# Kernel optimization log

Measured on AMD Instinct MI355X. Metric: run time of the kernel, lower is better.

## Reference

```python
import jax, jax.numpy as jnp
import numpy as np
from math import factorial, sqrt, pi

# ---- static config (matches init_kwargs) ----
C = 64            # channel multiplicity of hidden irreps 64x0e+64x1o+64x2e
L_HID = 2
MAX_ELL = 3
N_BASIS = 8
R_MAX = 5.0
AVG_NEI = 16.0
NUM_SPECIES = 5
N_NODES = 10000
N_EDGES = 160000
RAD_HID = 64
DIMS = [2 * l + 1 for l in range(L_HID + 1)]   # [1,3,5]

# ---- Clebsch-Gordan coefficients in the real spherical-harmonic basis ----
def _cg(j1, m1, j2, m2, j3, m3):
    if m1 + m2 != m3:
        return 0.0
    f = factorial
    pref = sqrt((2 * j3 + 1) * f(j3 + j1 - j2) * f(j3 - j1 + j2) * f(j1 + j2 - j3) / f(j1 + j2 + j3 + 1))
    pref *= sqrt(f(j3 + m3) * f(j3 - m3) * f(j1 - m1) * f(j1 + m1) * f(j2 - m2) * f(j2 + m2))
    s = 0.0
    for k in range(j1 + j2 - j3 + 1):
        d = (k, j1 + j2 - j3 - k, j1 - m1 - k, j2 + m2 - k, j3 - j2 + m1 + k, j3 - j1 - m2 + k)
        if min(d) < 0:
            continue
        s += (-1.0) ** k / np.prod([float(f(x)) for x in d])
    return pref * s

def _real_basis(l):
    A = np.zeros((2 * l + 1, 2 * l + 1), dtype=complex)
    for mp in range(-l, l + 1):
        if mp > 0:
            A[l + mp, l + mp] = (-1) ** mp / sqrt(2); A[l + mp, l - mp] = 1 / sqrt(2)
        elif mp == 0:
            A[l, l] = 1.0
        else:
            m = -mp
            A[l + mp, l - m] = 1j / sqrt(2); A[l + mp, l + m] = -1j * (-1) ** m / sqrt(2)
    return A

def _real_cg(l1, l2, l3):
    Cc = np.zeros((2 * l1 + 1, 2 * l2 + 1, 2 * l3 + 1), dtype=complex)
    for a in range(-l1, l1 + 1):
        for b in range(-l2, l2 + 1):
            c = a + b
            if -l3 <= c <= l3:
                Cc[l1 + a, l2 + b, l3 + c] = _cg(l1, a, l2, b, l3, c)
    A1, A2, A3 = _real_basis(l1), _real_basis(l2), _real_basis(l3)
    Cr = np.einsum('ia,jb,kc,abc->ijk', A1, A2, A3.conj(), Cc)
    R = Cr.real if np.abs(Cr.real).sum() >= np.abs(Cr.imag).sum() else Cr.imag
    R = R / max(np.sqrt((R ** 2).sum()), 1e-12)   # path-normalized
    return jnp.asarray(R.astype(np.float32))

def _paths(ls_in):
    ps = []
    for l1 in ls_in:
        for l2 in range(MAX_ELL + 1):
            for l3 in range(L_HID + 1):
                # triangle inequality + parity match (hidden parities are (-1)^l, SH parity (-1)^l)
                if abs(l1 - l2) <= l3 <= l1 + l2 and (l1 + l2 + l3) % 2 == 0:
                    ps.append((l1, l2, l3))
    return ps

PATHS = [_paths([0]), _paths(list(range(L_HID + 1)))]   # layer 0: 3 paths, layer 1: 13 paths
CG = {p: _real_cg(*p) for layer in PATHS for p in layer}

# ---- real spherical harmonics up to l=3 (component-style normalization) ----
def sph_harm(u):
    x, y, z = u[:, 0], u[:, 1], u[:, 2]
    Y0 = jnp.ones_like(x)[:, None]
    Y1 = sqrt(3.0) * jnp.stack([y, z, x], -1)
    Y2 = jnp.stack([sqrt(15) * x * y, sqrt(15) * y * z, sqrt(5) / 2 * (3 * z * z - 1),
                    sqrt(15) * x * z, sqrt(15) / 2 * (x * x - y * y)], -1)
    Y3 = jnp.stack([sqrt(35 / 8) * y * (3 * x * x - y * y), sqrt(105) * x * y * z,
                    sqrt(21 / 8) * y * (5 * z * z - 1), sqrt(7) / 2 * z * (5 * z * z - 3),
                    sqrt(21 / 8) * x * (5 * z * z - 1), sqrt(105) / 2 * z * (x * x - y * y),
                    sqrt(35 / 8) * x * (x * x - 3 * y * y)], -1)
    return [Y0, Y1, Y2, Y3]

def bessel(r):
    # e3nn.bessel(r, N_BASIS, R_MAX)
    n = jnp.arange(1, N_BASIS + 1, dtype=r.dtype)
    rs = jnp.maximum(r, 1e-6)[:, None]
    return sqrt(2.0 / R_MAX) * jnp.sin(n * pi * rs / R_MAX) / rs

def soft_envelope(r):
    # e3nn.soft_envelope: value_at_origin=1.2, arg_multiplicator=2.0
    t = 2.0 * (1.0 - r / R_MAX)
    sus = jnp.where(t > 0, jnp.exp(-1.0 / jnp.where(t > 0, t, 1.0)), 0.0)
    return (1.2 / np.exp(-0.5)) * sus

def interaction(h, Ys, rad, paths, rad_w1, rad_w2, mix, senders, receivers, n_nodes):
    # radial MLP -> per-path, per-channel tensor-product weights
    w = jax.nn.silu(rad @ rad_w1) @ rad_w2                       # [E, P*C]
    w = w.reshape(rad.shape[0], len(paths), C)
    hs = {l: h[l][senders] for l in {p[0] for p in paths}}       # gather once per input l
    acc = [None] * (L_HID + 1)
    for p, (l1, l2, l3) in enumerate(paths):
        # CG tensor product of sender features with edge spherical harmonics
        m = jnp.einsum('eci,ej,ijk,ec->eck', hs[l1], Ys[l2], CG[(l1, l2, l3)], w[:, p])
        acc[l3] = m if acc[l3] is None else acc[l3] + m
    out = {}
    for l in range(L_HID + 1):
        node_m = jax.ops.segment_sum(acc[l], receivers, num_segments=n_nodes) / AVG_NEI
        out[l] = jnp.einsum('nck,cd->ndk', node_m, mix[l])       # linear channel mixing per irrep
    return out

def forward(positions, w_embed, rad_w1_0, rad_w2_0, mix0, read0,
            rad_w1_1, rad_w2_1, mix1, skip1, read1, species, senders, receivers):
    n = positions.shape[0]
    rel = positions[receivers] - positions[senders]              # [E,3]
    r = jnp.sqrt(jnp.sum(rel * rel, -1) + 1e-12)
    u = rel / r[:, None]
    Ys = sph_harm(u)
    rad = bessel(r) * soft_envelope(r)[:, None]                  # [E,B]
    h = {0: w_embed[species][:, :, None]}                        # initial scalar node features
    # layer 0 (skip_connection_first_layer=False)
    h = interaction(h, Ys, rad, PATHS[0], rad_w1_0, rad_w2_0, mix0, senders, receivers, n)
    out0 = jnp.concatenate([jnp.einsum('nck,cd->ndk', h[l], read0[l]).reshape(n, -1)
                            for l in range(L_HID + 1)], -1)      # [N, C*9]
    # layer 1 (with linear skip connection)
    m = interaction(h, Ys, rad, PATHS[1], rad_w1_1, rad_w2_1, mix1, senders, receivers, n)
    h = {l: m[l] + jnp.einsum('nck,cd->ndk', h[l], skip1[l]) for l in range(L_HID + 1)}
    out1 = jnp.concatenate([jnp.einsum('nck,cd->ndk', h[l], read1[l]).reshape(n, -1)
                            for l in range(L_HID + 1)], -1)
    # per-layer readouts stacked then flattened == axis_to_mul over the layer axis
    return jnp.concatenate([out0, out1], -1)                     # [N, 2*C*9] = [N, 1152]

def setup_inputs() -> dict:
    key = jax.random.key(0)
    ks = jax.random.split(key, 14)
    P = [len(PATHS[0]), len(PATHS[1])]
    def w(k, shape, fan_in):
        return jax.random.normal(k, shape, jnp.float32) / np.sqrt(fan_in)
    return {
        'positions': jax.random.normal(ks[0], (N_NODES, 3), jnp.float32) * 1.5,
        'species': jax.random.randint(ks[1], (N_NODES,), 0, NUM_SPECIES),
        'senders': jax.random.randint(ks[2], (N_EDGES,), 0, N_NODES),
        'receivers': jax.random.randint(ks[3], (N_EDGES,), 0, N_NODES),
        'w_embed': w(ks[4], (NUM_SPECIES, C), 1),
        'rad_w1_0': w(ks[5], (N_BASIS, RAD_HID), N_BASIS),
        'rad_w2_0': w(ks[6], (RAD_HID, P[0] * C), RAD_HID),
        'mix0': w(ks[7], (L_HID + 1, C, C), C),
        'read0': w(ks[8], (L_HID + 1, C, C), C),
        'rad_w1_1': w(ks[9], (N_BASIS, RAD_HID), N_BASIS),
        'rad_w2_1': w(ks[10], (RAD_HID, P[1] * C), RAD_HID),
        'mix1': w(ks[11], (L_HID + 1, C, C), C),
        'skip1': w(ks[12], (L_HID + 1, C, C), C),
        'read1': w(ks[13], (L_HID + 1, C, C), C),
    }

def reference(positions, species, senders, receivers, w_embed, rad_w1_0, rad_w2_0, mix0, read0,
              rad_w1_1, rad_w2_1, mix1, skip1, read1):
    return forward(positions, w_embed, rad_w1_0, rad_w2_0, mix0, read0,
                   rad_w1_1, rad_w2_1, mix1, skip1, read1, species, senders, receivers)
```

## Files before the change

### kernel.cpp

```cpp
#include <hip/hip_runtime.h>
#include <math.h>

#define NE 160000
#define NN 10000
#define NP1 13
#define CG_TOTAL 573
#define CC_TOTAL 171
#define G_TOTAL 145
#define G1PAD 172
#define G0PAD 16

typedef __attribute__((ext_vector_type(8))) short bf16x8;
typedef __attribute__((ext_vector_type(4))) float f32x4;

constexpr int c_l1[NP1]   = {0,0,0,1,1,1,1,1,2,2,2,2,2};
constexpr int c_l2[NP1]   = {0,1,2,0,1,1,2,3,0,1,2,2,3};
constexpr int c_l3[NP1]   = {0,1,2,1,0,2,1,2,2,1,0,2,1};
constexpr int c_cgoff[NP1+1]= {0,1,10,35,44,53,98,143,248,273,318,343,468,573};
constexpr int c_ccoff[NP1+1]= {0,1,4,9,12,21,30,45,66,71,86,111,136,171};
constexpr int c_poff1[NP1] = {0,4,8,16,28,32,48,60,76,104,120,128,156};
constexpr int c_poff0[3]   = {0,4,8};
constexpr int YB[4] = {0,1,4,9};

__device__ float g_cg[640];
__device__ int   g_dec1[160];
__device__ int   g_dec0[16];
__device__ float g_ys[(size_t)NE*16];
__device__ float g_rad[(size_t)NE*8];
__device__ unsigned short g_hb0[(size_t)NE*64];
__device__ unsigned short g_hb1[(size_t)NE*64];
__device__ unsigned short g_Bp0[12*2*64*8];
__device__ unsigned short g_Bp1[52*2*64*8];
__device__ unsigned short g_W0[(size_t)NE*192];
__device__ unsigned short g_W1[(size_t)NE*832];
__device__ float g_G1[(size_t)NE*G1PAD];
__device__ float g_G0[(size_t)NE*G0PAD];
__device__ float g_acc0[(size_t)NN*576];
__device__ float g_acc1[(size_t)NN*576];
__device__ float g_h0[(size_t)NN*576];
__device__ int g_cnt[NN];
__device__ int g_cur[NN];
__device__ int g_off[NN+1];
__device__ int g_jof[NE];
__device__ int g_snds[NE];
__device__ int g_specs[NE];

__device__ inline unsigned short f2bf(float f){
  unsigned u = __float_as_uint(f);
  unsigned r = (u + 0x7FFFu + ((u>>16)&1u)) >> 16;
  return (unsigned short)r;
}
__device__ inline float bf2f(unsigned short h){ return __uint_as_float(((unsigned)h)<<16); }
__device__ inline float silu(float a){ return a/(1.f+expf(-a)); }

__device__ double dfact(int n){ double f=1.0; for(int i=2;i<=n;++i) f*=(double)i; return f; }

__device__ double cg_coef(int j1,int m1,int j2,int m2,int j3,int m3){
  if(m1+m2!=m3) return 0.0;
  double pref = sqrt((2.0*j3+1.0)*dfact(j3+j1-j2)*dfact(j3-j1+j2)*dfact(j1+j2-j3)/dfact(j1+j2+j3+1));
  pref *= sqrt(dfact(j3+m3)*dfact(j3-m3)*dfact(j1-m1)*dfact(j1+m1)*dfact(j2-m2)*dfact(j2+m2));
  double s=0.0;
  for(int k=0;k<=j1+j2-j3;++k){
    int d0=k, d1=j1+j2-j3-k, d2=j1-m1-k, d3=j2+m2-k, d4=j3-j2+m1+k, d5=j3-j1-m2+k;
    if(d1<0||d2<0||d3<0||d4<0||d5<0) continue;
    double denom = dfact(d0)*dfact(d1)*dfact(d2)*dfact(d3)*dfact(d4)*dfact(d5);
    s += ((k&1)? -1.0:1.0)/denom;
  }
  return pref*s;
}

__device__ inline void rb_elem(int l, int i, int j, double& re, double& im){
  re=0.0; im=0.0;
  int mp = i - l;
  const double is2 = 0.70710678118654752440;
  if(mp>0){
    if(j==l+mp) re = ((mp&1)? -1.0:1.0)*is2;
    else if(j==l-mp) re = is2;
  } else if(mp==0){
    if(j==l) re = 1.0;
  } else {
    int m=-mp;
    if(j==l-m) im = is2;
    else if(j==l+m) im = -(((m&1)?-1.0:1.0))*is2;
  }
}

__global__ __launch_bounds__(1024) void k_cg(){
  __shared__ double s_cc[CC_TOTAL];
  __shared__ double s_crr[CG_TOTAL];
  __shared__ double s_cri[CG_TOTAL];
  __shared__ double s_inv[NP1];
  __shared__ int    s_useR[NP1];
  int tid = threadIdx.x;

  if(tid==0){
    int r=0;
    for(int q=0;q<NP1;q++){
      int l2=c_l2[q], l3=c_l3[q];
      int d1=2*c_l1[q]+1, d2=2*l2+1, d3=2*l3+1;
      for(int i=0;i<d1;i++)for(int k=0;k<d3;k++){
        int cgs = c_cgoff[q] + i*d2*d3 + k;
        int dst = c_poff1[q] + i*d3 + k;
        g_dec1[r++] = cgs | (YB[l2]<<10) | (d2<<14) | (d3<<17) | (dst<<20);
      }
    }
    r=0;
    for(int q=0;q<3;q++){
      int l2=c_l2[q], l3=c_l3[q];
      int d2=2*l2+1, d3=2*l3+1;
      for(int k=0;k<d3;k++){
        int cgs = c_cgoff[q] + k;
        int dst = c_poff0[q] + k;
        g_dec0[r++] = cgs | (YB[l2]<<10) | (d2<<14) | (d3<<17) | (dst<<20);
      }
    }
  }

  if(tid < CC_TOTAL){
    int p=0; while(tid >= c_ccoff[p+1]) p++;
    int r = tid - c_ccoff[p];
    int l1=c_l1[p], l2=c_l2[p], l3=c_l3[p];
    int d2=2*l2+1;
    int ai = r/d2, bi = r - ai*d2;
    int a = ai - l1, b = bi - l2, c = a + b;
    double v = 0.0;
    if(c >= -l3 && c <= l3) v = cg_coef(l1,a,l2,b,l3,c);
    s_cc[tid] = v;
  }
  __syncthreads();

  if(tid < CG_TOTAL){
    int p=0; while(tid >= c_cgoff[p+1]) p++;
    int r = tid - c_cgoff[p];
    int l1=c_l1[p], l2=c_l2[p], l3=c_l3[p];
    int d2=2*l2+1, d3=2*l3+1;
    int i = r/(d2*d3), rem = r - i*(d2*d3);
    int j = rem/d3, k = rem - j*d3;
    double accr=0.0, acci=0.0;
    int d1=2*l1+1;
    for(int ai=0; ai<d1; ai++){
      double a1r,a1i; rb_elem(l1,i,ai,a1r,a1i);
      if(a1r==0.0 && a1i==0.0) continue;
      for(int bi=0; bi<d2; bi++){
        double cc = s_cc[c_ccoff[p] + ai*d2 + bi];
        if(cc==0.0) continue;
        int ci = (ai - l1) + (bi - l2) + l3;
        if(ci < 0 || ci >= d3) continue;
        double a2r,a2i; rb_elem(l2,j,bi,a2r,a2i);
        if(a2r==0.0 && a2i==0.0) continue;
        double a3r,a3i; rb_elem(l3,k,ci,a3r,a3i);
        a3i = -a3i;
        double p12r = a1r*a2r - a1i*a2i;
        double p12i = a1r*a2i + a1i*a2r;
        accr += (p12r*a3r - p12i*a3i)*cc;
        acci += (p12r*a3i + p12i*a3r)*cc;
      }
    }
    s_crr[tid] = accr;
    s_cri[tid] = acci;
  }
  __syncthreads();

  if(tid < NP1){
    int beg=c_cgoff[tid], end=c_cgoff[tid+1];
    double sr=0.0, si=0.0;
    for(int t=beg;t<end;t++){ sr += fabs(s_crr[t]); si += fabs(s_cri[t]); }
    int useR = (sr>=si);
    double nrm=0.0;
    for(int t=beg;t<end;t++){ double v = useR? s_crr[t] : s_cri[t]; nrm += v*v; }
    nrm = sqrt(nrm); if(nrm<1e-12) nrm=1e-12;
    s_useR[tid]=useR; s_inv[tid]=1.0/nrm;
  }
  __syncthreads();

  if(tid < CG_TOTAL){
    int p=0; while(tid >= c_cgoff[p+1]) p++;
    double v = s_useR[p]? s_crr[tid] : s_cri[tid];
    g_cg[tid] = (float)(v*s_inv[p]);
  }
}

__global__ void k_zero(){
  int i = blockIdx.x*256 + threadIdx.x;
  if(i<NN){ g_cnt[i]=0; g_cur[i]=0; }
}

__global__ void k_hist(const int* __restrict__ rcv){
  int e = blockIdx.x*256 + threadIdx.x;
  if(e<NE) atomicAdd(&g_cnt[rcv[e]], 1);
}

__global__ void k_scan(){
  __shared__ int lds[1024];
  int t = threadIdx.x;
  int base = t*10;
  int s = 0;
  for(int i=0;i<10;i++){ int idx=base+i; if(idx<NN) s += g_cnt[idx]; }
  lds[t]=s; __syncthreads();
  for(int o=1;o<1024;o<<=1){
    int v = (t>=o)? lds[t-o] : 0;
    __syncthreads();
    lds[t]+=v;
    __syncthreads();
  }
  int run = lds[t]-s;
  for(int i=0;i<10;i++){ int idx=base+i; if(idx<NN){ g_off[idx]=run; run+=g_cnt[idx]; } }
  if(t==0) g_off[NN]=NE;
}

__global__ void k_scatter(const int* __restrict__ rcv, const int* __restrict__ snd,
                          const int* __restrict__ spec){
  int e = blockIdx.x*256 + threadIdx.x;
  if(e<NE){
    int r = rcv[e];
    int p = atomicAdd(&g_cur[r],1);
    int j = g_off[r]+p;
    g_jof[e] = j;
    int s = snd[e];
    g_snds[j] = s;
    g_specs[j] = spec[s];
  }
}

__global__ void k_edge(const float* __restrict__ pos, const int* __restrict__ snd,
                       const int* __restrict__ rcv){
  int e = blockIdx.x*blockDim.x + threadIdx.x;
  if(e>=NE) return;
  int s=snd[e], r=rcv[e];
  int j=g_jof[e];
  float dx=pos[r*3+0]-pos[s*3+0];
  float dy=pos[r*3+1]-pos[s*3+1];
  float dz=pos[r*3+2]-pos[s*3+2];
  float rr = sqrtf(dx*dx+dy*dy+dz*dz + 1e-12f);
  float x=dx/rr, y=dy/rr, z=dz/rr;
  float Y[16];
  Y[0]=1.f;
  const float s3=1.7320508075688772f;
  Y[1]=s3*y; Y[2]=s3*z; Y[3]=s3*x;
  const float s15=3.872983346207417f;
  const float s5h=1.118033988749895f;
  Y[4]=s15*x*y; Y[5]=s15*y*z; Y[6]=s5h*(3.f*z*z-1.f); Y[7]=s15*x*z; Y[8]=0.5f*s15*(x*x-y*y);
  const float s35_8=2.0916500663351889f;
  const float s105=10.246950765959598f;
  const float s21_8=1.6201851746019651f;
  const float s7h=1.3228756555322954f;
  Y[9]=s35_8*y*(3.f*x*x-y*y);
  Y[10]=s105*x*y*z;
  Y[11]=s21_8*y*(5.f*z*z-1.f);
  Y[12]=s7h*z*(5.f*z*z-3.f);
  Y[13]=s21_8*x*(5.f*z*z-1.f);
  Y[14]=0.5f*s105*z*(x*x-y*y);
  Y[15]=s35_8*x*(x*x-3.f*y*y);
  #pragma unroll
  for(int i=0;i<16;i++) g_ys[(size_t)j*16+i]=Y[i];
  float t = 2.f*(1.f - rr*0.2f);
  float env = (t>0.f)? 1.9784655248401538f*expf(-1.f/t) : 0.f;
  float rs = fmaxf(rr,1e-6f);
  const float sq25 = 0.6324555320336759f;
  float pre = sq25/rs * env;
  const float pi5 = 0.6283185307179586f;
  #pragma unroll
  for(int b=0;b<8;b++){
    g_rad[(size_t)j*8+b] = pre * sinf((float)(b+1)*pi5*rs);
  }
}

__global__ __launch_bounds__(256) void k_gbuild(){
  __shared__ float cg[CG_TOTAL];
  __shared__ int dec1[G_TOTAL];
  __shared__ int dec0[9];
  __shared__ __align__(16) float Yl[4][8][17];
  __shared__ __align__(16) float Gl[4][8][G1PAD];
  __shared__ __align__(16) float G0l[4][8][G0PAD];
  int tid=threadIdx.x;
  for(int t=tid;t<CG_TOTAL;t+=256) cg[t]=g_cg[t];
  for(int t=tid;t<G_TOTAL;t+=256) dec1[t]=g_dec1[t];
  if(tid<9) dec0[tid]=g_dec0[tid];
  __syncthreads();
  const int lane=tid&63, wid=tid>>6;
  const int e0=blockIdx.x*32 + wid*8;
  #pragma unroll
  for(int t=lane;t<128;t+=64){
    int r=t>>4, c=t&15;
    Yl[wid][r][c]=g_ys[(size_t)(e0+r)*16+c];
  }
  asm volatile("s_waitcnt lgkmcnt(0)" ::: "memory");
  for(int s=0;s<19;s++){
    int idx = lane + 64*s;
    if(idx<1160){
      int e = idx/145, r = idx - 145*e;
      int d = dec1[r];
      int cgs=d&1023, yb=(d>>10)&15, d2=(d>>14)&7, d3n=(d>>17)&7, dst=(d>>20)&255;
      float g=0.f;
      for(int jj=0;jj<d2;jj++) g += Yl[wid][e][yb+jj]*cg[cgs+jj*d3n];
      Gl[wid][e][dst]=g;
    }
  }
  for(int idx=lane; idx<72; idx+=64){
    int e = idx/9, r = idx - 9*e;
    int d = dec0[r];
    int cgs=d&1023, yb=(d>>10)&15, d2=(d>>14)&7, d3n=(d>>17)&7, dst=(d>>20)&255;
    float g=0.f;
    for(int jj=0;jj<d2;jj++) g += Yl[wid][e][yb+jj]*cg[cgs+jj*d3n];
    G0l[wid][e][dst]=g;
  }
  asm volatile("s_waitcnt lgkmcnt(0)" ::: "memory");
  {
    f32x4* dst=(f32x4*)&g_G1[(size_t)e0*G1PAD];
    const f32x4* src=(const f32x4*)&Gl[wid][0][0];
    for(int t=lane;t<344;t+=64) dst[t]=src[t];
  }
  {
    f32x4* dst=(f32x4*)&g_G0[(size_t)e0*G0PAD];
    const f32x4* src=(const f32x4*)&G0l[wid][0][0];
    if(lane<32) dst[lane]=src[lane];
  }
}

__global__ __launch_bounds__(256) void k_hidden(const float* __restrict__ W1a,
                                                const float* __restrict__ W1b){
  int idx = blockIdx.x*256 + threadIdx.x;
  int c = idx & 63;
  const float* rd = &g_rad[(size_t)(idx>>6)*8];
  float a0=0.f, a1=0.f;
  #pragma unroll
  for(int b=0;b<8;b++){
    float rv = rd[b];
    a0 += rv*W1a[b*64+c];
    a1 += rv*W1b[b*64+c];
  }
  g_hb0[idx] = f2bf(silu(a0));
  g_hb1[idx] = f2bf(silu(a1));
}

template<int NCOLS>
__global__ void k_repack(const float* __restrict__ W2){
  constexpr int NCB = NCOLS/16;
  int t = blockIdx.x*256 + threadIdx.x;
  if(t >= NCB*128) return;
  int cb = t>>7, rest = t&127, ks = rest>>6, l = rest&63;
  int col = cb*16 + (l&15);
  unsigned short* dst = (NCOLS==832)? g_Bp1 : g_Bp0;
  #pragma unroll
  for(int j=0;j<8;j++){
    int k = ks*32 + ((l>>4)<<3) + j;
    dst[(size_t)t*8+j] = f2bf(W2[k*NCOLS + col]);
  }
}

template<int NCOLS>
__global__ __launch_bounds__(256) void k_wgemm(){
  constexpr int NCB = NCOLS/16;
  const unsigned short* hb = (NCOLS==832)? g_hb1 : g_hb0;
  const unsigned short* Bp = (NCOLS==832)? g_Bp1 : g_Bp0;
  unsigned short* W = (NCOLS==832)? g_W1 : g_W0;
  const int lane = threadIdx.x & 63;
  const int wid  = threadIdx.x >> 6;
  const int e0 = blockIdx.x*128 + wid*32;
  const int rowl = lane & 15, kg = lane >> 4;
  bf16x8 a[2][2];
  #pragma unroll
  for(int mr=0;mr<2;mr++){
    #pragma unroll
    for(int ks=0;ks<2;ks++){
      a[mr][ks] = *reinterpret_cast<const bf16x8*>(&hb[(size_t)(e0+mr*16+rowl)*64 + ks*32 + kg*8]);
    }
  }
  for(int cb=0;cb<NCB;cb++){
    bf16x8 b0 = *reinterpret_cast<const bf16x8*>(&Bp[((size_t)(cb*2+0)*64+lane)*8]);
    bf16x8 b1 = *reinterpret_cast<const bf16x8*>(&Bp[((size_t)(cb*2+1)*64+lane)*8]);
    #pragma unroll
    for(int mr=0;mr<2;mr++){
      f32x4 acc = {0.f,0.f,0.f,0.f};
      acc = __builtin_amdgcn_mfma_f32_16x16x32_bf16(a[mr][0], b0, acc, 0,0,0);
      acc = __builtin_amdgcn_mfma_f32_16x16x32_bf16(a[mr][1], b1, acc, 0,0,0);
      #pragma unroll
      for(int r=0;r<4;r++){
        int row = kg*4 + r;
        W[(size_t)(e0+mr*16+row)*NCOLS + cb*16 + rowl] = f2bf(acc[r]);
      }
    }
  }
}

__global__ __launch_bounds__(256) void k_gather0(const float* __restrict__ wemb){
  const int lane=threadIdx.x&63, wid=threadIdx.x>>6;
  const int n=blockIdx.x*4+wid;
  const int beg=__builtin_amdgcn_readfirstlane(g_off[n]);
  const int end=__builtin_amdgcn_readfirstlane(g_off[n+1]);
  float acc[9];
  #pragma unroll
  for(int k=0;k<9;k++) acc[k]=0.f;
  for(int j=beg;j<end;j++){
    const float* Ge=&g_G0[(size_t)j*G0PAD];
    f32x4 qa=*reinterpret_cast<const f32x4*>(Ge+0);
    f32x4 qb=*reinterpret_cast<const f32x4*>(Ge+4);
    f32x4 qc=*reinterpret_cast<const f32x4*>(Ge+8);
    f32x4 qd=*reinterpret_cast<const f32x4*>(Ge+12);
    int sp=__builtin_amdgcn_readfirstlane(g_specs[j]);
    float hs=wemb[sp*64+lane];
    const unsigned short* wp=&g_W0[(size_t)j*192 + lane];
    float a0=bf2f(wp[0])*hs, a1=bf2f(wp[64])*hs, a2=bf2f(wp[128])*hs;
    acc[0]+=a0*qa[0];
    acc[1]+=a1*qb[0]; acc[2]+=a1*qb[1]; acc[3]+=a1*qb[2];
    acc[4]+=a2*qc[0]; acc[5]+=a2*qc[1]; acc[6]+=a2*qc[2]; acc[7]+=a2*qc[3];
    acc[8]+=a2*qd[0];
  }
  #pragma unroll
  for(int k=0;k<9;k++) g_acc0[(size_t)n*576 + k*64 + lane]=acc[k];
}

#define DP(P_,L1_,L3_,OFF_) { \
  constexpr int d1_=2*(L1_)+1, d3_=2*(L3_)+1, ib_=(L1_)*(L1_), kb_=(L3_)*(L3_); \
  constexpr int nv_=((d1_*d3_)+3)/4; \
  f32x4 gq[nv_]; \
  _Pragma("unroll") \
  for(int q_=0;q_<nv_;q_++) gq[q_]=*reinterpret_cast<const f32x4*>(Ge+(OFF_)+4*q_); \
  _Pragma("unroll") \
  for(int k_=0;k_<d3_;k_++){ \
    float tk_=0.f; \
    _Pragma("unroll") \
    for(int i_=0;i_<d1_;i_++){ tk_+=h[ib_+i_]*gq[(i_*d3_+k_)>>2][(i_*d3_+k_)&3]; } \
    acc[kb_+k_]+=w[P_]*tk_; } }

__global__ __launch_bounds__(256) void k_gather1(){
  const int lane=threadIdx.x&63, wid=threadIdx.x>>6;
  const int n=blockIdx.x*4+wid;
  const int beg=__builtin_amdgcn_readfirstlane(g_off[n]);
  const int end=__builtin_amdgcn_readfirstlane(g_off[n+1]);
  float acc[9];
  #pragma unroll
  for(int k=0;k<9;k++) acc[k]=0.f;
  for(int j=beg;j<end;j++){
    const int s=__builtin_amdgcn_readfirstlane(g_snds[j]);
    const float* Ge=&g_G1[(size_t)j*G1PAD];
    float h[9];
    #pragma unroll
    for(int i=0;i<9;i++) h[i]=g_h0[(size_t)s*576 + i*64 + lane];
    const unsigned short* wp=&g_W1[(size_t)j*832 + lane];
    float w[13];
    #pragma unroll
    for(int p=0;p<13;p++) w[p]=bf2f(wp[p*64]);
    DP(0,0,0,0)
    DP(1,0,1,4)
    DP(2,0,2,8)
    DP(3,1,1,16)
    DP(4,1,0,28)
    DP(5,1,2,32)
    DP(6,1,1,48)
    DP(7,1,2,60)
    DP(8,2,2,76)
    DP(9,2,1,104)
    DP(10,2,0,120)
    DP(11,2,2,128)
    DP(12,2,1,156)
  }
  #pragma unroll
  for(int k=0;k<9;k++) g_acc1[(size_t)n*576 + k*64 + lane]=acc[k];
}

__global__ __launch_bounds__(256) void k_node0(const float* __restrict__ mix,
    const float* __restrict__ read, float* __restrict__ out){
  __shared__ float nm[4][9][64];
  __shared__ float hl[4][9][64];
  int lane=threadIdx.x&63, wid=threadIdx.x>>6;
  int n=blockIdx.x*4+wid;
  #pragma unroll
  for(int kk=0;kk<9;kk++) nm[wid][kk][lane]=g_acc0[(size_t)n*576+kk*64+lane]*(1.f/16.f);
  asm volatile("s_waitcnt lgkmcnt(0)" ::: "memory");
  float h[9];
  #pragma unroll
  for(int kk=0;kk<9;kk++) h[kk]=0.f;
  for(int c=0;c<64;c++){
    float m0=mix[c*64+lane], m1=mix[4096+c*64+lane], m2=mix[8192+c*64+lane];
    h[0]+=nm[wid][0][c]*m0;
    #pragma unroll
    for(int k=0;k<3;k++) h[1+k]+=nm[wid][1+k][c]*m1;
    #pragma unroll
    for(int k=0;k<5;k++) h[4+k]+=nm[wid][4+k][c]*m2;
  }
  #pragma unroll
  for(int kk=0;kk<9;kk++){ g_h0[(size_t)n*576+kk*64+lane]=h[kk]; hl[wid][kk][lane]=h[kk]; }
  asm volatile("s_waitcnt lgkmcnt(0)" ::: "memory");
  float o[9];
  #pragma unroll
  for(int kk=0;kk<9;kk++) o[kk]=0.f;
  for(int c=0;c<64;c++){
    float r0=read[c*64+lane], r1=read[4096+c*64+lane], r2=read[8192+c*64+lane];
    o[0]+=hl[wid][0][c]*r0;
    #pragma unroll
    for(int k=0;k<3;k++) o[1+k]+=hl[wid][1+k][c]*r1;
    #pragma unroll
    for(int k=0;k<5;k++) o[4+k]+=hl[wid][4+k][c]*r2;
  }
  float* op=&out[(size_t)n*1152];
  op[lane]=o[0];
  #pragma unroll
  for(int k=0;k<3;k++) op[64 + lane*3+k]=o[1+k];
  #pragma unroll
  for(int k=0;k<5;k++) op[256 + lane*5+k]=o[4+k];
}

__global__ __launch_bounds__(256) void k_node1(const float* __restrict__ mix,
    const float* __restrict__ skip, const float* __restrict__ read, float* __restrict__ out){
  __shared__ float nm[4][9][64];
  __shared__ float h0l[4][9][64];
  __shared__ float hn[4][9][64];
  int lane=threadIdx.x&63, wid=threadIdx.x>>6;
  int n=blockIdx.x*4+wid;
  #pragma unroll
  for(int kk=0;kk<9;kk++){
    nm[wid][kk][lane]=g_acc1[(size_t)n*576+kk*64+lane]*(1.f/16.f);
    h0l[wid][kk][lane]=g_h0[(size_t)n*576+kk*64+lane];
  }
  asm volatile("s_waitcnt lgkmcnt(0)" ::: "memory");
  float h[9];
  #pragma unroll
  for(int kk=0;kk<9;kk++) h[kk]=0.f;
  for(int c=0;c<64;c++){
    float m0=mix[c*64+lane], m1=mix[4096+c*64+lane], m2=mix[8192+c*64+lane];
    float s0=skip[c*64+lane], s1=skip[4096+c*64+lane], s2=skip[8192+c*64+lane];
    h[0]+=nm[wid][0][c]*m0 + h0l[wid][0][c]*s0;
    #pragma unroll
    for(int k=0;k<3;k++) h[1+k]+=nm[wid][1+k][c]*m1 + h0l[wid][1+k][c]*s1;
    #pragma unroll
    for(int k=0;k<5;k++) h[4+k]+=nm[wid][4+k][c]*m2 + h0l[wid][4+k][c]*s2;
  }
  #pragma unroll
  for(int kk=0;kk<9;kk++) hn[wid][kk][lane]=h[kk];
  asm volatile("s_waitcnt lgkmcnt(0)" ::: "memory");
  float o[9];
  #pragma unroll
  for(int kk=0;kk<9;kk++) o[kk]=0.f;
  for(int c=0;c<64;c++){
    float r0=read[c*64+lane], r1=read[4096+c*64+lane], r2=read[8192+c*64+lane];
    o[0]+=hn[wid][0][c]*r0;
    #pragma unroll
    for(int k=0;k<3;k++) o[1+k]+=hn[wid][1+k][c]*r1;
    #pragma unroll
    for(int k=0;k<5;k++) o[4+k]+=hn[wid][4+k][c]*r2;
  }
  float* op=&out[(size_t)n*1152 + 576];
  op[lane]=o[0];
  #pragma unroll
  for(int k=0;k<3;k++) op[64 + lane*3+k]=o[1+k];
  #pragma unroll
  for(int k=0;k<5;k++) op[256 + lane*5+k]=o[4+k];
}

extern "C" void kernel_launch(void* const* d_in, const int* in_sizes, int n_in,
                              void* d_out, int out_size, void* d_ws, size_t ws_size,
                              hipStream_t stream) {
  (void)in_sizes; (void)n_in; (void)out_size; (void)d_ws; (void)ws_size;
  const float* pos  =(const float*)d_in[0];
  const int*   spec =(const int*)  d_in[1];
  const int*   snd  =(const int*)  d_in[2];
  const int*   rcv  =(const int*)  d_in[3];
  const float* wemb =(const float*)d_in[4];
  const float* w1_0 =(const float*)d_in[5];
  const float* w2_0 =(const float*)d_in[6];
  const float* mix0 =(const float*)d_in[7];
  const float* read0=(const float*)d_in[8];
  const float* w1_1 =(const float*)d_in[9];
  const float* w2_1 =(const float*)d_in[10];
  const float* mix1 =(const float*)d_in[11];
  const float* skip1=(const float*)d_in[12];
  const float* read1=(const float*)d_in[13];
  float* out=(float*)d_out;

  k_cg<<<1,1024,0,stream>>>();
  k_zero<<<(NN+255)/256,256,0,stream>>>();
  k_hist<<<NE/256,256,0,stream>>>(rcv);
  k_scan<<<1,1024,0,stream>>>();
  k_scatter<<<NE/256,256,0,stream>>>(rcv,snd,spec);
  k_edge<<<(NE+255)/256,256,0,stream>>>(pos,snd,rcv);
  k_gbuild<<<NE/32,256,0,stream>>>();
  k_hidden<<<NE*64/256,256,0,stream>>>(w1_0,w1_1);
  k_repack<192><<<6,256,0,stream>>>(w2_0);
  k_repack<832><<<26,256,0,stream>>>(w2_1);
  k_wgemm<192><<<NE/128,256,0,stream>>>();
  k_wgemm<832><<<NE/128,256,0,stream>>>();
  k_gather0<<<NN/4,256,0,stream>>>(wemb);
  k_node0<<<NN/4,256,0,stream>>>(mix0,read0,out);
  k_gather1<<<NN/4,256,0,stream>>>();
  k_node1<<<NN/4,256,0,stream>>>(mix1,skip1,read1,out);
}
```

Measured before the change: 745.8 us.

## Split gather work into fixed-size edge chunks and store geometry tensors in bf16

Gather kernels now iterate over 16-edge chunks from a global work list using persistent grids. Nodes spanning several chunks accumulate with atomic adds into pre-zeroed accumulators. The per-edge CG-contracted geometry tensors G0/G1 are stored as bf16 packed vectors instead of fp32, which roughly halves their memory traffic. This adds a zeroing pass over both accumulators, float atomics, and some precision loss from rounding G to bf16.

```diff
diff --git a/kernel.cpp b/kernel.cpp
--- a/kernel.cpp
+++ b/kernel.cpp
@@ -7,10 +7,12 @@
 #define CG_TOTAL 573
 #define CC_TOTAL 171
 #define G_TOTAL 145
-#define G1PAD 172
-#define G0PAD 16
+#define G1B 200
+#define G0B 24
+#define MAXCHUNK 32768
 
 typedef __attribute__((ext_vector_type(8))) short bf16x8;
+typedef __attribute__((ext_vector_type(8))) unsigned short u16x8;
 typedef __attribute__((ext_vector_type(4))) float f32x4;
 
 constexpr int c_l1[NP1]   = {0,0,0,1,1,1,1,1,2,2,2,2,2};
@@ -18,8 +20,8 @@
 constexpr int c_l3[NP1]   = {0,1,2,1,0,2,1,2,2,1,0,2,1};
 constexpr int c_cgoff[NP1+1]= {0,1,10,35,44,53,98,143,248,273,318,343,468,573};
 constexpr int c_ccoff[NP1+1]= {0,1,4,9,12,21,30,45,66,71,86,111,136,171};
-constexpr int c_poff1[NP1] = {0,4,8,16,28,32,48,60,76,104,120,128,156};
-constexpr int c_poff0[3]   = {0,4,8};
+constexpr int c_poff1b[NP1] = {0,8,16,24,40,48,64,80,96,128,144,152,184};
+constexpr int c_poff0b[3]   = {0,8,16};
 constexpr int YB[4] = {0,1,4,9};
 
 __device__ float g_cg[640];
@@ -33,8 +35,8 @@
 __device__ unsigned short g_Bp1[52*2*64*8];
 __device__ unsigned short g_W0[(size_t)NE*192];
 __device__ unsigned short g_W1[(size_t)NE*832];
-__device__ float g_G1[(size_t)NE*G1PAD];
-__device__ float g_G0[(size_t)NE*G0PAD];
+__device__ unsigned short g_G1b[(size_t)NE*G1B];
+__device__ unsigned short g_G0b[(size_t)NE*G0B];
 __device__ float g_acc0[(size_t)NN*576];
 __device__ float g_acc1[(size_t)NN*576];
 __device__ float g_h0[(size_t)NN*576];
@@ -44,6 +46,8 @@
 __device__ int g_jof[NE];
 __device__ int g_snds[NE];
 __device__ int g_specs[NE];
+__device__ int2 g_chunk[MAXCHUNK];
+__device__ int g_nchunks;
 
 __device__ inline unsigned short f2bf(float f){
   unsigned u = __float_as_uint(f);
@@ -100,7 +104,7 @@
       int d1=2*c_l1[q]+1, d2=2*l2+1, d3=2*l3+1;
       for(int i=0;i<d1;i++)for(int k=0;k<d3;k++){
         int cgs = c_cgoff[q] + i*d2*d3 + k;
-        int dst = c_poff1[q] + i*d3 + k;
+        int dst = c_poff1b[q] + i*d3 + k;
         g_dec1[r++] = cgs | (YB[l2]<<10) | (d2<<14) | (d3<<17) | (dst<<20);
       }
     }
@@ -110,7 +114,7 @@
       int d2=2*l2+1, d3=2*l3+1;
       for(int k=0;k<d3;k++){
         int cgs = c_cgoff[q] + k;
-        int dst = c_poff0[q] + k;
+        int dst = c_poff0b[q] + k;
         g_dec0[r++] = cgs | (YB[l2]<<10) | (d2<<14) | (d3<<17) | (dst<<20);
       }
     }
@@ -181,8 +185,10 @@
 }
 
 __global__ void k_zero(){
-  int i = blockIdx.x*256 + threadIdx.x;
+  size_t i = (size_t)blockIdx.x*256 + threadIdx.x;
   if(i<NN){ g_cnt[i]=0; g_cur[i]=0; }
+  if(i==NN) g_nchunks=0;
+  if(i < (size_t)NN*576){ g_acc0[i]=0.f; g_acc1[i]=0.f; }
 }
 
 __global__ void k_hist(const int* __restrict__ rcv){
@@ -206,6 +212,21 @@
   int run = lds[t]-s;
   for(int i=0;i<10;i++){ int idx=base+i; if(idx<NN){ g_off[idx]=run; run+=g_cnt[idx]; } }
   if(t==0) g_off[NN]=NE;
+}
+
+__global__ void k_chunks(){
+  int n = blockIdx.x*256 + threadIdx.x;
+  if(n>=NN) return;
+  int beg = g_off[n];
+  int deg = g_off[n+1]-beg;
+  int nch = (deg+15)>>4;
+  if(!nch) return;
+  int base = atomicAdd(&g_nchunks, nch);
+  int pb = (nch>1)? (1<<20) : 0;
+  for(int c=0;c<nch;c++){
+    int cnt = min(16, deg-16*c);
+    g_chunk[base+c] = make_int2(n | (cnt<<14) | pb, beg+16*c);
+  }
 }
 
 __global__ void k_scatter(const int* __restrict__ rcv, const int* __restrict__ snd,
@@ -270,8 +291,8 @@
   __shared__ int dec1[G_TOTAL];
   __shared__ int dec0[9];
   __shared__ __align__(16) float Yl[4][8][17];
-  __shared__ __align__(16) float Gl[4][8][G1PAD];
-  __shared__ __align__(16) float G0l[4][8][G0PAD];
+  __shared__ __align__(16) float Gl[4][8][G1B];
+  __shared__ __align__(16) float G0l[4][8][G0B];
   int tid=threadIdx.x;
   for(int t=tid;t<CG_TOTAL;t+=256) cg[t]=g_cg[t];
   for(int t=tid;t<G_TOTAL;t+=256) dec1[t]=g_dec1[t];
@@ -305,15 +326,21 @@
     G0l[wid][e][dst]=g;
   }
   asm volatile("s_waitcnt lgkmcnt(0)" ::: "memory");
-  {
-    f32x4* dst=(f32x4*)&g_G1[(size_t)e0*G1PAD];
-    const f32x4* src=(const f32x4*)&Gl[wid][0][0];
-    for(int t=lane;t<344;t+=64) dst[t]=src[t];
-  }
-  {
-    f32x4* dst=(f32x4*)&g_G0[(size_t)e0*G0PAD];
-    const f32x4* src=(const f32x4*)&G0l[wid][0][0];
-    if(lane<32) dst[lane]=src[lane];
+  for(int t=lane;t<200;t+=64){
+    int e=t/25, v=t-25*e;
+    const float* src=&Gl[wid][e][v*8];
+    u16x8 pk;
+    #pragma unroll
+    for(int i=0;i<8;i++) pk[i]=f2bf(src[i]);
+    *(reinterpret_cast<u16x8*>(&g_G1b[(size_t)(e0+e)*G1B]) + v) = pk;
+  }
+  for(int t=lane;t<24;t+=64){
+    int e=t/3, v=t-3*e;
+    const float* src=&G0l[wid][e][v*8];
+    u16x8 pk;
+    #pragma unroll
+    for(int i=0;i<8;i++) pk[i]=f2bf(src[i]);
+    *(reinterpret_cast<u16x8*>(&g_G0b[(size_t)(e0+e)*G0B]) + v) = pk;
   }
 }
 
@@ -383,80 +410,108 @@
   }
 }
 
-__global__ __launch_bounds__(256) void k_gather0(const float* __restrict__ wemb){
-  const int lane=threadIdx.x&63, wid=threadIdx.x>>6;
-  const int n=blockIdx.x*4+wid;
-  const int beg=__builtin_amdgcn_readfirstlane(g_off[n]);
-  const int end=__builtin_amdgcn_readfirstlane(g_off[n+1]);
-  float acc[9];
-  #pragma unroll
-  for(int k=0;k<9;k++) acc[k]=0.f;
-  for(int j=beg;j<end;j++){
-    const float* Ge=&g_G0[(size_t)j*G0PAD];
-    f32x4 qa=*reinterpret_cast<const f32x4*>(Ge+0);
-    f32x4 qb=*reinterpret_cast<const f32x4*>(Ge+4);
-    f32x4 qc=*reinterpret_cast<const f32x4*>(Ge+8);
-    f32x4 qd=*reinterpret_cast<const f32x4*>(Ge+12);
-    int sp=__builtin_amdgcn_readfirstlane(g_specs[j]);
-    float hs=wemb[sp*64+lane];
-    const unsigned short* wp=&g_W0[(size_t)j*192 + lane];
-    float a0=bf2f(wp[0])*hs, a1=bf2f(wp[64])*hs, a2=bf2f(wp[128])*hs;
-    acc[0]+=a0*qa[0];
-    acc[1]+=a1*qb[0]; acc[2]+=a1*qb[1]; acc[3]+=a1*qb[2];
-    acc[4]+=a2*qc[0]; acc[5]+=a2*qc[1]; acc[6]+=a2*qc[2]; acc[7]+=a2*qc[3];
-    acc[8]+=a2*qd[0];
-  }
-  #pragma unroll
-  for(int k=0;k<9;k++) g_acc0[(size_t)n*576 + k*64 + lane]=acc[k];
-}
-
-#define DP(P_,L1_,L3_,OFF_) { \
+__device__ __forceinline__ void pedge0(int j, int lane, float acc[9], const float* __restrict__ wemb){
+  const int sp = g_specs[j];
+  const u16x8* Gp = reinterpret_cast<const u16x8*>(&g_G0b[(size_t)j*G0B]);
+  u16x8 q0=Gp[0], q1=Gp[1], q2=Gp[2];
+  const unsigned short* wp=&g_W0[(size_t)j*192 + lane];
+  float w0=bf2f(wp[0]), w1=bf2f(wp[64]), w2=bf2f(wp[128]);
+  float hs=wemb[sp*64+lane];
+  float a0=w0*hs, a1=w1*hs, a2=w2*hs;
+  acc[0]+=a0*bf2f(q0[0]);
+  acc[1]+=a1*bf2f(q1[0]); acc[2]+=a1*bf2f(q1[1]); acc[3]+=a1*bf2f(q1[2]);
+  acc[4]+=a2*bf2f(q2[0]); acc[5]+=a2*bf2f(q2[1]); acc[6]+=a2*bf2f(q2[2]);
+  acc[7]+=a2*bf2f(q2[3]); acc[8]+=a2*bf2f(q2[4]);
+}
+
+#define DP(P_,L1_,L3_,V0_) { \
   constexpr int d1_=2*(L1_)+1, d3_=2*(L3_)+1, ib_=(L1_)*(L1_), kb_=(L3_)*(L3_); \
-  constexpr int nv_=((d1_*d3_)+3)/4; \
-  f32x4 gq[nv_]; \
+  constexpr int nv_=((d1_*d3_)+7)/8; \
+  u16x8 gv_[nv_]; \
   _Pragma("unroll") \
-  for(int q_=0;q_<nv_;q_++) gq[q_]=*reinterpret_cast<const f32x4*>(Ge+(OFF_)+4*q_); \
+  for(int q_=0;q_<nv_;q_++) gv_[q_]=Gp[(V0_)+q_]; \
   _Pragma("unroll") \
   for(int k_=0;k_<d3_;k_++){ \
     float tk_=0.f; \
     _Pragma("unroll") \
-    for(int i_=0;i_<d1_;i_++){ tk_+=h[ib_+i_]*gq[(i_*d3_+k_)>>2][(i_*d3_+k_)&3]; } \
+    for(int i_=0;i_<d1_;i_++){ tk_+=h[ib_+i_]*bf2f(gv_[(i_*d3_+k_)>>3][(i_*d3_+k_)&7]); } \
     acc[kb_+k_]+=w[P_]*tk_; } }
 
-__global__ __launch_bounds__(256) void k_gather1(){
+__device__ __forceinline__ void pedge1(int j, int lane, float acc[9]){
+  const int s = g_snds[j];
+  const u16x8* Gp = reinterpret_cast<const u16x8*>(&g_G1b[(size_t)j*G1B]);
+  const unsigned short* wp = &g_W1[(size_t)j*832 + lane];
+  float w[13];
+  #pragma unroll
+  for(int p=0;p<13;p++) w[p]=bf2f(wp[p*64]);
+  float h[9];
+  #pragma unroll
+  for(int i=0;i<9;i++) h[i]=g_h0[(size_t)s*576 + i*64 + lane];
+  DP(0,0,0,0)
+  DP(1,0,1,1)
+  DP(2,0,2,2)
+  DP(3,1,1,3)
+  DP(4,1,0,5)
+  DP(5,1,2,6)
+  DP(6,1,1,8)
+  DP(7,1,2,10)
+  DP(8,2,2,12)
+  DP(9,2,1,16)
+  DP(10,2,0,18)
+  DP(11,2,2,19)
+  DP(12,2,1,23)
+}
+
+__global__ __launch_bounds__(256,2) void k_gather0(const float* __restrict__ wemb){
   const int lane=threadIdx.x&63, wid=threadIdx.x>>6;
-  const int n=blockIdx.x*4+wid;
-  const int beg=__builtin_amdgcn_readfirstlane(g_off[n]);
-  const int end=__builtin_amdgcn_readfirstlane(g_off[n+1]);
-  float acc[9];
-  #pragma unroll
-  for(int k=0;k<9;k++) acc[k]=0.f;
-  for(int j=beg;j<end;j++){
-    const int s=__builtin_amdgcn_readfirstlane(g_snds[j]);
-    const float* Ge=&g_G1[(size_t)j*G1PAD];
-    float h[9];
-    #pragma unroll
-    for(int i=0;i<9;i++) h[i]=g_h0[(size_t)s*576 + i*64 + lane];
-    const unsigned short* wp=&g_W1[(size_t)j*832 + lane];
-    float w[13];
-    #pragma unroll
-    for(int p=0;p<13;p++) w[p]=bf2f(wp[p*64]);
-    DP(0,0,0,0)
-    DP(1,0,1,4)
-    DP(2,0,2,8)
-    DP(3,1,1,16)
-    DP(4,1,0,28)
-    DP(5,1,2,32)
-    DP(6,1,1,48)
-    DP(7,1,2,60)
-    DP(8,2,2,76)
-    DP(9,2,1,104)
-    DP(10,2,0,120)
-    DP(11,2,2,128)
-    DP(12,2,1,156)
-  }
-  #pragma unroll
-  for(int k=0;k<9;k++) g_acc1[(size_t)n*576 + k*64 + lane]=acc[k];
+  const int NC = g_nchunks;
+  for(int c = blockIdx.x*4+wid; c < NC; c += gridDim.x*4){
+    const int2 ch = g_chunk[c];
+    const int n = ch.x & 0x3FFF;
+    const int cnt = (ch.x>>14) & 31;
+    const int partial = (ch.x>>20) & 1;
+    const int j0 = ch.y;
+    float acc[9];
+    #pragma unroll
+    for(int k=0;k<9;k++) acc[k]=0.f;
+    int t=0;
+    for(; t+1<cnt; t+=2){ pedge0(j0+t,lane,acc,wemb); pedge0(j0+t+1,lane,acc,wemb); }
+    if(t<cnt) pedge0(j0+t,lane,acc,wemb);
+    float* ap=&g_acc0[(size_t)n*576 + lane];
+    if(partial){
+      #pragma unroll
+      for(int k=0;k<9;k++) unsafeAtomicAdd(ap+k*64, acc[k]);
+    } else {
+      #pragma unroll
+      for(int k=0;k<9;k++) ap[k*64]=acc[k];
+    }
+  }
+}
+
+__global__ __launch_bounds__(256,2) void k_gather1(){
+  const int lane=threadIdx.x&63, wid=threadIdx.x>>6;
+  const int NC = g_nchunks;
+  for(int c = blockIdx.x*4+wid; c < NC; c += gridDim.x*4){
+    const int2 ch = g_chunk[c];
+    const int n = ch.x & 0x3FFF;
+    const int cnt = (ch.x>>14) & 31;
+    const int partial = (ch.x>>20) & 1;
+    const int j0 = ch.y;
+    float acc[9];
+    #pragma unroll
+    for(int k=0;k<9;k++) acc[k]=0.f;
+    int t=0;
+    for(; t+1<cnt; t+=2){ pedge1(j0+t,lane,acc); pedge1(j0+t+1,lane,acc); }
+    if(t<cnt) pedge1(j0+t,lane,acc);
+    float* ap=&g_acc1[(size_t)n*576 + lane];
+    if(partial){
+      #pragma unroll
+      for(int k=0;k<9;k++) unsafeAtomicAdd(ap+k*64, acc[k]);
+    } else {
+      #pragma unroll
+      for(int k=0;k<9;k++) ap[k*64]=acc[k];
+    }
+  }
 }
 
 __global__ __launch_bounds__(256) void k_node0(const float* __restrict__ mix,
@@ -569,9 +624,10 @@
   float* out=(float*)d_out;
 
   k_cg<<<1,1024,0,stream>>>();
-  k_zero<<<(NN+255)/256,256,0,stream>>>();
+  k_zero<<<(NN*576+255)/256,256,0,stream>>>();
   k_hist<<<NE/256,256,0,stream>>>(rcv);
   k_scan<<<1,1024,0,stream>>>();
+  k_chunks<<<(NN+255)/256,256,0,stream>>>();
   k_scatter<<<NE/256,256,0,stream>>>(rcv,snd,spec);
   k_edge<<<(NE+255)/256,256,0,stream>>>(pos,snd,rcv);
   k_gbuild<<<NE/32,256,0,stream>>>();
@@ -580,8 +636,8 @@
   k_repack<832><<<26,256,0,stream>>>(w2_1);
   k_wgemm<192><<<NE/128,256,0,stream>>>();
   k_wgemm<832><<<NE/128,256,0,stream>>>();
-  k_gather0<<<NN/4,256,0,stream>>>(wemb);
+  k_gather0<<<512,256,0,stream>>>(wemb);
   k_node0<<<NN/4,256,0,stream>>>(mix0,read0,out);
-  k_gather1<<<NN/4,256,0,stream>>>();
+  k_gather1<<<512,256,0,stream>>>();
   k_node1<<<NN/4,256,0,stream>>>(mix1,skip1,read1,out);
 }
```

Result: slower. 996.7 us (+33.6%).

## Balance gather work with 16-edge chunks, atomics, prefetching and transposed h0

Applied to the files above, without the earlier changes.

The per-node gather loops are replaced by a persistent grid that walks a list of 16-edge chunks built from the CSR offsets. Nodes with more than one chunk combine their partial sums with float atomics into pre-zeroed accumulators. Each chunk loop double-buffers the next edge's loads, and h0 is also stored transposed so a lane fetches its 9 values in three vector loads. This targets load imbalance from uneven node degrees and load latency, at the cost of an extra chunk-building kernel, zeroing the accumulators, atomic traffic and a second copy of h0.

```diff
diff --git a/kernel.cpp b/kernel.cpp
--- a/kernel.cpp
+++ b/kernel.cpp
@@ -9,8 +9,10 @@
 #define G_TOTAL 145
 #define G1PAD 172
 #define G0PAD 16
+#define MAXCHUNK 32768
 
 typedef __attribute__((ext_vector_type(8))) short bf16x8;
+typedef __attribute__((ext_vector_type(8))) unsigned short u16x8;
 typedef __attribute__((ext_vector_type(4))) float f32x4;
 
 constexpr int c_l1[NP1]   = {0,0,0,1,1,1,1,1,2,2,2,2,2};
@@ -38,12 +40,15 @@
 __device__ float g_acc0[(size_t)NN*576];
 __device__ float g_acc1[(size_t)NN*576];
 __device__ float g_h0[(size_t)NN*576];
+__device__ float g_h0t[(size_t)NN*64*12];
 __device__ int g_cnt[NN];
 __device__ int g_cur[NN];
 __device__ int g_off[NN+1];
 __device__ int g_jof[NE];
 __device__ int g_snds[NE];
 __device__ int g_specs[NE];
+__device__ int2 g_chunk[MAXCHUNK];
+__device__ int g_nchunks;
 
 __device__ inline unsigned short f2bf(float f){
   unsigned u = __float_as_uint(f);
@@ -181,8 +186,10 @@
 }
 
 __global__ void k_zero(){
-  int i = blockIdx.x*256 + threadIdx.x;
+  size_t i = (size_t)blockIdx.x*256 + threadIdx.x;
   if(i<NN){ g_cnt[i]=0; g_cur[i]=0; }
+  if(i==NN) g_nchunks=0;
+  if(i < (size_t)NN*576){ g_acc0[i]=0.f; g_acc1[i]=0.f; }
 }
 
 __global__ void k_hist(const int* __restrict__ rcv){
@@ -206,6 +213,21 @@
   int run = lds[t]-s;
   for(int i=0;i<10;i++){ int idx=base+i; if(idx<NN){ g_off[idx]=run; run+=g_cnt[idx]; } }
   if(t==0) g_off[NN]=NE;
+}
+
+__global__ void k_chunks(){
+  int n = blockIdx.x*256 + threadIdx.x;
+  if(n>=NN) return;
+  int beg = g_off[n];
+  int deg = g_off[n+1]-beg;
+  int nch = (deg+15)>>4;
+  if(!nch) return;
+  int base = atomicAdd(&g_nchunks, nch);
+  int pb = (nch>1)? (1<<20) : 0;
+  for(int c=0;c<nch;c++){
+    int cnt = min(16, deg-16*c);
+    g_chunk[base+c] = make_int2(n | (cnt<<14) | pb, beg+16*c);
+  }
 }
 
 __global__ void k_scatter(const int* __restrict__ rcv, const int* __restrict__ snd,
@@ -383,31 +405,34 @@
   }
 }
 
-__global__ __launch_bounds__(256) void k_gather0(const float* __restrict__ wemb){
-  const int lane=threadIdx.x&63, wid=threadIdx.x>>6;
-  const int n=blockIdx.x*4+wid;
-  const int beg=__builtin_amdgcn_readfirstlane(g_off[n]);
-  const int end=__builtin_amdgcn_readfirstlane(g_off[n+1]);
-  float acc[9];
-  #pragma unroll
-  for(int k=0;k<9;k++) acc[k]=0.f;
-  for(int j=beg;j<end;j++){
-    const float* Ge=&g_G0[(size_t)j*G0PAD];
-    f32x4 qa=*reinterpret_cast<const f32x4*>(Ge+0);
-    f32x4 qb=*reinterpret_cast<const f32x4*>(Ge+4);
-    f32x4 qc=*reinterpret_cast<const f32x4*>(Ge+8);
-    f32x4 qd=*reinterpret_cast<const f32x4*>(Ge+12);
-    int sp=__builtin_amdgcn_readfirstlane(g_specs[j]);
-    float hs=wemb[sp*64+lane];
-    const unsigned short* wp=&g_W0[(size_t)j*192 + lane];
-    float a0=bf2f(wp[0])*hs, a1=bf2f(wp[64])*hs, a2=bf2f(wp[128])*hs;
-    acc[0]+=a0*qa[0];
-    acc[1]+=a1*qb[0]; acc[2]+=a1*qb[1]; acc[3]+=a1*qb[2];
-    acc[4]+=a2*qc[0]; acc[5]+=a2*qc[1]; acc[6]+=a2*qc[2]; acc[7]+=a2*qc[3];
-    acc[8]+=a2*qd[0];
-  }
-  #pragma unroll
-  for(int k=0;k<9;k++) g_acc0[(size_t)n*576 + k*64 + lane]=acc[k];
+struct EB0 { unsigned short w0,w1,w2; float hs; };
+struct EB1 { unsigned short w[13]; f32x4 h0,h1,h2; };
+
+__device__ __forceinline__ void load0(EB0& b, int j, int sp, int lane, const float* __restrict__ wemb){
+  const unsigned short* wp=&g_W0[(size_t)j*192 + lane];
+  b.w0=wp[0]; b.w1=wp[64]; b.w2=wp[128];
+  b.hs=wemb[sp*64+lane];
+}
+
+__device__ __forceinline__ void comp0(const EB0& b, int j, float acc[9]){
+  const float* Ge=&g_G0[(size_t)j*G0PAD];
+  f32x4 qa=*reinterpret_cast<const f32x4*>(Ge+0);
+  f32x4 qb=*reinterpret_cast<const f32x4*>(Ge+4);
+  f32x4 qc=*reinterpret_cast<const f32x4*>(Ge+8);
+  f32x4 qd=*reinterpret_cast<const f32x4*>(Ge+12);
+  float a0=bf2f(b.w0)*b.hs, a1=bf2f(b.w1)*b.hs, a2=bf2f(b.w2)*b.hs;
+  acc[0]+=a0*qa[0];
+  acc[1]+=a1*qb[0]; acc[2]+=a1*qb[1]; acc[3]+=a1*qb[2];
+  acc[4]+=a2*qc[0]; acc[5]+=a2*qc[1]; acc[6]+=a2*qc[2]; acc[7]+=a2*qc[3];
+  acc[8]+=a2*qd[0];
+}
+
+__device__ __forceinline__ void load1(EB1& b, int j, int s, int lane){
+  const unsigned short* wp=&g_W1[(size_t)j*832 + lane];
+  #pragma unroll
+  for(int p=0;p<13;p++) b.w[p]=wp[p*64];
+  const f32x4* hp=reinterpret_cast<const f32x4*>(&g_h0t[((size_t)s*64+lane)*12]);
+  b.h0=hp[0]; b.h1=hp[1]; b.h2=hp[2];
 }
 
 #define DP(P_,L1_,L3_,OFF_) { \
@@ -423,40 +448,96 @@
     for(int i_=0;i_<d1_;i_++){ tk_+=h[ib_+i_]*gq[(i_*d3_+k_)>>2][(i_*d3_+k_)&3]; } \
     acc[kb_+k_]+=w[P_]*tk_; } }
 
+__device__ __forceinline__ void comp1(const EB1& b, int j, float acc[9]){
+  const float* Ge=&g_G1[(size_t)j*G1PAD];
+  float w[13];
+  #pragma unroll
+  for(int p=0;p<13;p++) w[p]=bf2f(b.w[p]);
+  float h[9];
+  h[0]=b.h0[0]; h[1]=b.h0[1]; h[2]=b.h0[2]; h[3]=b.h0[3];
+  h[4]=b.h1[0]; h[5]=b.h1[1]; h[6]=b.h1[2]; h[7]=b.h1[3];
+  h[8]=b.h2[0];
+  DP(0,0,0,0)
+  DP(1,0,1,4)
+  DP(2,0,2,8)
+  DP(3,1,1,16)
+  DP(4,1,0,28)
+  DP(5,1,2,32)
+  DP(6,1,1,48)
+  DP(7,1,2,60)
+  DP(8,2,2,76)
+  DP(9,2,1,104)
+  DP(10,2,0,120)
+  DP(11,2,2,128)
+  DP(12,2,1,156)
+}
+
+__global__ __launch_bounds__(256) void k_gather0(const float* __restrict__ wemb){
+  const int lane=threadIdx.x&63, wid=threadIdx.x>>6;
+  const int NC = g_nchunks;
+  for(int c = blockIdx.x*4+wid; c < NC; c += gridDim.x*4){
+    const int2 ch = g_chunk[c];
+    const int n = ch.x & 0x3FFF;
+    const int cnt = (ch.x>>14) & 31;
+    const int partial = (ch.x>>20) & 1;
+    const int j0 = ch.y;
+    int spv = g_specs[j0 + ((lane<cnt)? lane : 0)];
+    float acc[9];
+    #pragma unroll
+    for(int k=0;k<9;k++) acc[k]=0.f;
+    EB0 A,B;
+    load0(A, j0, __shfl(spv,0), lane, wemb);
+    int t=0;
+    for(; t+2<=cnt; t+=2){
+      load0(B, j0+t+1, __shfl(spv,t+1), lane, wemb);
+      comp0(A, j0+t, acc);
+      if(t+2<cnt) load0(A, j0+t+2, __shfl(spv,t+2), lane, wemb);
+      comp0(B, j0+t+1, acc);
+    }
+    if(t<cnt) comp0(A, j0+t, acc);
+    float* ap=&g_acc0[(size_t)n*576 + lane];
+    if(partial){
+      #pragma unroll
+      for(int k=0;k<9;k++) unsafeAtomicAdd(ap+k*64, acc[k]);
+    } else {
+      #pragma unroll
+      for(int k=0;k<9;k++) ap[k*64]=acc[k];
+    }
+  }
+}
+
 __global__ __launch_bounds__(256) void k_gather1(){
   const int lane=threadIdx.x&63, wid=threadIdx.x>>6;
-  const int n=blockIdx.x*4+wid;
-  const int beg=__builtin_amdgcn_readfirstlane(g_off[n]);
-  const int end=__builtin_amdgcn_readfirstlane(g_off[n+1]);
-  float acc[9];
-  #pragma unroll
-  for(int k=0;k<9;k++) acc[k]=0.f;
-  for(int j=beg;j<end;j++){
-    const int s=__builtin_amdgcn_readfirstlane(g_snds[j]);
-    const float* Ge=&g_G1[(size_t)j*G1PAD];
-    float h[9];
-    #pragma unroll
-    for(int i=0;i<9;i++) h[i]=g_h0[(size_t)s*576 + i*64 + lane];
-    const unsigned short* wp=&g_W1[(size_t)j*832 + lane];
-    float w[13];
-    #pragma unroll
-    for(int p=0;p<13;p++) w[p]=bf2f(wp[p*64]);
-    DP(0,0,0,0)
-    DP(1,0,1,4)
-    DP(2,0,2,8)
-    DP(3,1,1,16)
-    DP(4,1,0,28)
-    DP(5,1,2,32)
-    DP(6,1,1,48)
-    DP(7,1,2,60)
-    DP(8,2,2,76)
-    DP(9,2,1,104)
-    DP(10,2,0,120)
-    DP(11,2,2,128)
-    DP(12,2,1,156)
-  }
-  #pragma unroll
-  for(int k=0;k<9;k++) g_acc1[(size_t)n*576 + k*64 + lane]=acc[k];
+  const int NC = g_nchunks;
+  for(int c = blockIdx.x*4+wid; c < NC; c += gridDim.x*4){
+    const int2 ch = g_chunk[c];
+    const int n = ch.x & 0x3FFF;
+    const int cnt = (ch.x>>14) & 31;
+    const int partial = (ch.x>>20) & 1;
+    const int j0 = ch.y;
+    int sv = g_snds[j0 + ((lane<cnt)? lane : 0)];
+    float acc[9];
+    #pragma unroll
+    for(int k=0;k<9;k++) acc[k]=0.f;
+    EB1 A,B;
+    load1(A, j0, __shfl(sv,0), lane);
+    int t=0;
+    for(; t+2<=cnt; t+=2){
+      load1(B, j0+t+1, __shfl(sv,t+1), lane);
+      comp1(A, j0+t, acc);
+      if(t+2<cnt) load1(A, j0+t+2, __shfl(sv,t+2), lane);
+      comp1(B, j0+t+1, acc);
+    }
+    if(t<cnt) comp1(A, j0+t, acc);
+    float* ap=&g_acc1[(size_t)n*576 + lane];
+    if(partial){
+      #pragma unroll
+      for(int k=0;k<9;k++) unsafeAtomicAdd(ap+k*64, acc[k]);
+    } else {
+      #pragma unroll
+      for(int k=0;k<9;k++) ap[k*64]=acc[k];
+    }
+  }
 }
 
 __global__ __launch_bounds__(256) void k_node0(const float* __restrict__ mix,
@@ -481,6 +562,15 @@
   }
   #pragma unroll
   for(int kk=0;kk<9;kk++){ g_h0[(size_t)n*576+kk*64+lane]=h[kk]; hl[wid][kk][lane]=h[kk]; }
+  {
+    float* hp=&g_h0t[((size_t)n*64+lane)*12];
+    f32x4 v0={h[0],h[1],h[2],h[3]};
+    f32x4 v1={h[4],h[5],h[6],h[7]};
+    f32x4 v2={h[8],0.f,0.f,0.f};
+    *reinterpret_cast<f32x4*>(hp)=v0;
+    *reinterpret_cast<f32x4*>(hp+4)=v1;
+    *reinterpret_cast<f32x4*>(hp+8)=v2;
+  }
   asm volatile("s_waitcnt lgkmcnt(0)" ::: "memory");
   float o[9];
   #pragma unroll
@@ -569,9 +659,10 @@
   float* out=(float*)d_out;
 
   k_cg<<<1,1024,0,stream>>>();
-  k_zero<<<(NN+255)/256,256,0,stream>>>();
+  k_zero<<<(NN*576+255)/256,256,0,stream>>>();
   k_hist<<<NE/256,256,0,stream>>>(rcv);
   k_scan<<<1,1024,0,stream>>>();
+  k_chunks<<<(NN+255)/256,256,0,stream>>>();
   k_scatter<<<NE/256,256,0,stream>>>(rcv,snd,spec);
   k_edge<<<(NE+255)/256,256,0,stream>>>(pos,snd,rcv);
   k_gbuild<<<NE/32,256,0,stream>>>();
@@ -580,8 +671,8 @@
   k_repack<832><<<26,256,0,stream>>>(w2_1);
   k_wgemm<192><<<NE/128,256,0,stream>>>();
   k_wgemm<832><<<NE/128,256,0,stream>>>();
-  k_gather0<<<NN/4,256,0,stream>>>(wemb);
+  k_gather0<<<4096,256,0,stream>>>(wemb);
   k_node0<<<NN/4,256,0,stream>>>(mix0,read0,out);
-  k_gather1<<<NN/4,256,0,stream>>>();
+  k_gather1<<<4096,256,0,stream>>>();
   k_node1<<<NN/4,256,0,stream>>>(mix1,skip1,read1,out);
 }
```

New measurement: 894.3 us. +19.9%, slower.
